# Performance work log

Hardware: AMD Instinct MI355X
Metric: run time of the kernel (lower is better)

## Reference

```python
import jax, jax.numpy as jnp
import numpy as np

HIDDEN = 1024
NUM_HEADS = 16
HEAD_DIM = HIDDEN // NUM_HEADS
GRID_SIZE = 5
SPLINE_ORDER = 3
NUM_COEF = GRID_SIZE + SPLINE_ORDER  # 8


def make_grid(in_features):
    # efficient-kan default grid: range [-1, 1], extended by spline_order on each side
    h = 2.0 / GRID_SIZE
    g = jnp.arange(-SPLINE_ORDER, GRID_SIZE + SPLINE_ORDER + 1, dtype=jnp.float32) * h - 1.0
    return jnp.broadcast_to(g, (in_features, g.shape[0]))  # (in, G+2k+1)


def b_splines(x, grid):
    # x: (N, in); grid: (in, G+2k+1) -> bases (N, in, G+k)
    x = x[..., None]
    bases = ((x >= grid[:, :-1]) & (x < grid[:, 1:])).astype(x.dtype)
    for k in range(1, SPLINE_ORDER + 1):
        left = (x - grid[:, : -(k + 1)]) / (grid[:, k:-1] - grid[:, : -(k + 1)])
        right = (grid[:, k + 1 :] - x) / (grid[:, k + 1 :] - grid[:, 1:-k])
        bases = left * bases[..., :-1] + right * bases[..., 1:]
    return bases


def kan_linear(x, base_w, spline_w, spline_scaler):
    # x: (..., in); base_w: (out, in); spline_w: (out, in, C); spline_scaler: (out, in)
    in_f = x.shape[-1]
    x2 = x.reshape(-1, in_f)
    base = jax.nn.silu(x2) @ base_w.T
    bases = b_splines(x2, make_grid(in_f))                      # (N, in, C)
    sw = spline_w * spline_scaler[..., None]                    # (out, in, C)
    spline = bases.reshape(x2.shape[0], -1) @ sw.reshape(sw.shape[0], -1).T
    return (base + spline).reshape(*x.shape[:-1], base_w.shape[0])


def apply_rope(x):
    # x: (B, H, S, D); interleaved rotary (lucidrains convention), theta=10000
    d, s = x.shape[-1], x.shape[-2]
    inv_freq = 1.0 / (10000.0 ** (jnp.arange(0, d, 2, dtype=jnp.float32) / d))
    freqs = jnp.arange(s, dtype=jnp.float32)[:, None] * inv_freq[None, :]  # (S, d/2)
    cos = jnp.repeat(jnp.cos(freqs), 2, axis=-1)
    sin = jnp.repeat(jnp.sin(freqs), 2, axis=-1)
    x1, x2 = x[..., 0::2], x[..., 1::2]
    rot = jnp.stack((-x2, x1), axis=-1).reshape(x.shape)
    return x * cos + rot * sin


def setup_inputs() -> dict:
    key = jax.random.key(0)
    ks = jax.random.split(key, 10)
    B, S, H = 2, 2048, HIDDEN
    H3 = 3 * H
    scale = 0.02
    return {
        "q": jax.random.normal(ks[0], (B, S, H), jnp.float32),
        "k": jax.random.normal(ks[1], (B, S, H), jnp.float32),
        "v": jax.random.normal(ks[2], (B, S, H), jnp.float32),
        "attn_mask": jnp.zeros((S, S), jnp.float32),
        "qkv_base_w": jax.random.normal(ks[3], (H3, H3), jnp.float32) * scale,
        "qkv_spline_w": jax.random.normal(ks[4], (H3, H3, NUM_COEF), jnp.float32) * scale,
        "qkv_scaler": jnp.ones((H3, H3), jnp.float32),
        "out_base_w": jax.random.normal(ks[5], (H, H), jnp.float32) * scale,
        "out_spline_w": jax.random.normal(ks[6], (H, H, NUM_COEF), jnp.float32) * scale,
        "out_scaler": jnp.ones((H, H), jnp.float32),
    }


def reference(q, k, v, attn_mask, qkv_base_w, qkv_spline_w, qkv_scaler,
              out_base_w, out_spline_w, out_scaler):
    B, S, H = q.shape
    x = jnp.concatenate((q, k, v), axis=2)                       # (B, S, 3H)
    qkv = kan_linear(x, qkv_base_w, qkv_spline_w, qkv_scaler)    # (B, S, 3H)
    qkv = qkv.reshape(B, S, NUM_HEADS, 3 * HEAD_DIM).transpose(0, 2, 1, 3)
    queries, keys, values = jnp.split(qkv, 3, axis=-1)           # each (B, nh, S, hd)
    queries = apply_rope(queries)
    keys = apply_rope(keys)
    scores = jnp.einsum("bhqd,bhkd->bhqk", queries, keys) / (HEAD_DIM ** 0.5) + attn_mask
    attention = jax.nn.softmax(scores, axis=-1)
    context = jnp.einsum("bhqk,bhkd->bhqd", attention, values)
    context = context.transpose(0, 2, 1, 3).reshape(B, S, H)
    return kan_linear(context, out_base_w, out_spline_w, out_scaler)
```

## Files before the change

### kernel.cpp

```cpp
#include <hip/hip_runtime.h>
#include <hip/hip_bf16.h>
#include <stdint.h>

typedef __bf16 bf16;
typedef __attribute__((ext_vector_type(8))) __bf16 bf16x8;
typedef __attribute__((ext_vector_type(4))) float f32x4;

#define DEVI __device__ __forceinline__

constexpr int BATCH = 2, SEQ = 2048, HID = 1024, NHEAD = 16, HDIM = 64;
constexpr int H3 = 3072;
constexpr int MROWS = BATCH * SEQ;
constexpr int KEXP = 9;
constexpr int K1DIM = H3 * KEXP;
constexpr int K2DIM = HID * KEXP;

constexpr size_t WQ_OFF  = 0;
constexpr size_t AQ_OFF  = 169869312;
constexpr size_t CQ_OFF  = AQ_OFF + 226492416;
constexpr size_t QR_OFF  = CQ_OFF + 50331648;
constexpr size_t KR_OFF  = QR_OFF + 8388608;
constexpr size_t VB_OFF  = KR_OFF + 8388608;
constexpr size_t CTX_OFF = VB_OFF + 8388608;
constexpr size_t A2_OFF  = 0;
constexpr size_t W2_OFF  = 75497472;

DEVI void gld_lds16(const void* g, void* l) {
  __builtin_amdgcn_global_load_lds((const __attribute__((address_space(1))) void*)g,
                                   (__attribute__((address_space(3))) void*)l, 16, 0, 0);
}

DEVI void silu_bases(float x, float* o9) {
  o9[0] = x / (1.0f + __expf(-x));
  float g[12];
#pragma unroll
  for (int j = 0; j < 12; ++j) g[j] = (float)(j - 3) * 0.4f - 1.0f;
  float b[11];
#pragma unroll
  for (int j = 0; j < 11; ++j) b[j] = (x >= g[j] && x < g[j + 1]) ? 1.0f : 0.0f;
#pragma unroll
  for (int k = 1; k <= 3; ++k) {
    const float inv = (k == 1) ? 2.5f : (k == 2) ? 1.25f : (1.0f / 1.2f);
#pragma unroll
    for (int j = 0; j + k < 11; ++j) {
      b[j] = (x - g[j]) * inv * b[j] + (g[j + k + 1] - x) * inv * b[j + 1];
    }
  }
#pragma unroll
  for (int c = 0; c < 8; ++c) o9[1 + c] = b[c];
}

__global__ void wprep_kernel(const float* __restrict__ bw, const float* __restrict__ sw,
                             const float* __restrict__ sc, bf16* __restrict__ W, int KK) {
  int i = blockIdx.x * blockDim.x + threadIdx.x;
  int n = blockIdx.y;
  if (i >= KK) return;
  size_t idx = (size_t)n * KK + i;
  float base = bw[idx];
  float scal = sc[idx];
  const float4* sp = (const float4*)(sw + idx * 8);
  float4 s0 = sp[0], s1 = sp[1];
  bf16* o = W + idx * KEXP;
  o[0] = (bf16)base;
  o[1] = (bf16)(s0.x * scal); o[2] = (bf16)(s0.y * scal);
  o[3] = (bf16)(s0.z * scal); o[4] = (bf16)(s0.w * scal);
  o[5] = (bf16)(s1.x * scal); o[6] = (bf16)(s1.y * scal);
  o[7] = (bf16)(s1.z * scal); o[8] = (bf16)(s1.w * scal);
}

__global__ void act_qkv_kernel(const float* __restrict__ qin, const float* __restrict__ kin,
                               const float* __restrict__ vin, bf16* __restrict__ A) {
  int i = blockIdx.x * blockDim.x + threadIdx.x;
  int m = blockIdx.y;
  int which = i >> 10, off = i & 1023;
  const float* src = (which == 0) ? qin : (which == 1) ? kin : vin;
  float x = src[(size_t)m * HID + off];
  float o9[9];
  silu_bases(x, o9);
  bf16* o = A + (size_t)m * K1DIM + (size_t)i * KEXP;
#pragma unroll
  for (int c = 0; c < 9; ++c) o[c] = (bf16)o9[c];
}

__global__ void act_out_kernel(const float* __restrict__ ctx, bf16* __restrict__ A) {
  int i = blockIdx.x * blockDim.x + threadIdx.x;
  int m = blockIdx.y;
  float x = ctx[(size_t)m * HID + i];
  float o9[9];
  silu_bases(x, o9);
  bf16* o = A + (size_t)m * K2DIM + (size_t)i * KEXP;
#pragma unroll
  for (int c = 0; c < 9; ++c) o[c] = (bf16)o9[c];
}

__global__ __launch_bounds__(256, 2)
void gemm_kernel(const bf16* __restrict__ A, const bf16* __restrict__ Bw,
                 float* __restrict__ C, int N, int K) {
  __shared__ bf16 As[128 * 64];
  __shared__ bf16 Bs[128 * 64];
  const int tid = threadIdx.x;
  const int lane = tid & 63;
  const int l15 = lane & 15, lq = lane >> 4;
  const int wid = tid >> 6;
  const int wm = (wid >> 1) * 64, wn = (wid & 1) * 64;
  const int bm = blockIdx.y, bn = blockIdx.x;
  f32x4 acc[4][4] = {};
  const int srow = tid >> 3;
  const int schk = (tid & 7) ^ (srow & 7);
  const bf16* aB = A + (size_t)(bm * 128 + srow) * K + schk * 8;
  const bf16* bB = Bw + (size_t)(bn * 128 + srow) * K + schk * 8;

  int aoff[2][4], boff[2][4];
#pragma unroll
  for (int ks = 0; ks < 2; ++ks) {
#pragma unroll
    for (int f = 0; f < 4; ++f) {
      int arow = wm + f * 16 + l15;
      int brow = wn + f * 16 + l15;
      aoff[ks][f] = arow * 64 + (((ks * 4 + lq) ^ (arow & 7)) * 8);
      boff[ks][f] = brow * 64 + (((ks * 4 + lq) ^ (brow & 7)) * 8);
    }
  }

  for (int kt = 0; kt < K; kt += 64) {
#pragma unroll
    for (int r = 0; r < 4; ++r) {
      gld_lds16(aB + (size_t)(r * 32) * K + kt, As + r * 2048 + tid * 8);
      gld_lds16(bB + (size_t)(r * 32) * K + kt, Bs + r * 2048 + tid * 8);
    }
    __syncthreads();
#pragma unroll
    for (int ks = 0; ks < 2; ++ks) {
      bf16x8 af[4], bfr[4];
#pragma unroll
      for (int mf = 0; mf < 4; ++mf)
        af[mf] = *(const bf16x8*)&As[aoff[ks][mf]];
#pragma unroll
      for (int nf = 0; nf < 4; ++nf)
        bfr[nf] = *(const bf16x8*)&Bs[boff[ks][nf]];
#pragma unroll
      for (int mf = 0; mf < 4; ++mf)
#pragma unroll
        for (int nf = 0; nf < 4; ++nf)
          acc[mf][nf] = __builtin_amdgcn_mfma_f32_16x16x32_bf16(af[mf], bfr[nf], acc[mf][nf], 0, 0, 0);
    }
    __syncthreads();
  }
#pragma unroll
  for (int mf = 0; mf < 4; ++mf)
#pragma unroll
    for (int nf = 0; nf < 4; ++nf)
#pragma unroll
      for (int r = 0; r < 4; ++r) {
        int row = bm * 128 + wm + mf * 16 + lq * 4 + r;
        int col = bn * 128 + wn + nf * 16 + l15;
        C[(size_t)row * N + col] = acc[mf][nf][r];
      }
}

__global__ void rope_kernel(const float* __restrict__ Cq, bf16* __restrict__ qr,
                            bf16* __restrict__ kr, bf16* __restrict__ vb) {
  int idx = blockIdx.x * blockDim.x + threadIdx.x;
  int p = idx & 31;
  int h = (idx >> 5) & 15;
  int m = idx >> 9;
  int s = m & (SEQ - 1);
  int b = m >> 11;
  const float* row = Cq + (size_t)m * H3 + h * 192;
  float q0 = row[2 * p], q1 = row[2 * p + 1];
  float k0 = row[64 + 2 * p], k1 = row[64 + 2 * p + 1];
  float v0 = row[128 + 2 * p], v1 = row[128 + 2 * p + 1];
  float invf = expf(-(float)p * (9.210340371976184f / 32.0f));
  float fr = (float)s * invf;
  float sn, cs;
  sincosf(fr, &sn, &cs);
  size_t o = (((size_t)(b * NHEAD + h)) * SEQ + s) * 64 + 2 * p;
  qr[o] = (bf16)(q0 * cs - q1 * sn); qr[o + 1] = (bf16)(q1 * cs + q0 * sn);
  kr[o] = (bf16)(k0 * cs - k1 * sn); kr[o + 1] = (bf16)(k1 * cs + k0 * sn);
  vb[o] = (bf16)v0; vb[o + 1] = (bf16)v1;
}

__global__ __launch_bounds__(256, 2)
void attn_kernel(const bf16* __restrict__ qr, const bf16* __restrict__ kr,
                 const bf16* __restrict__ vb, const float* __restrict__ mask,
                 float* __restrict__ ctx) {
  __shared__ bf16 Kt[64 * 64];
  __shared__ bf16 Vt[64 * 64];
  __shared__ bf16 Pl[4][16 * 64];
  const int tid = threadIdx.x, lane = tid & 63, wid = tid >> 6;
  const int l15 = lane & 15, lq = lane >> 4;
  const int qt = blockIdx.x, bh = blockIdx.y;
  const int b = bh >> 4, hh = bh & 15;
  const size_t baseQ = ((size_t)bh * SEQ + qt * 64 + wid * 16) * 64;
  bf16x8 aq[2];
  aq[0] = *(const bf16x8*)&qr[baseQ + (size_t)l15 * 64 + 0 + lq * 8];
  aq[1] = *(const bf16x8*)&qr[baseQ + (size_t)l15 * 64 + 32 + lq * 8];
  float mrow[4], lrow[4];
  f32x4 oacc[4] = {};
#pragma unroll
  for (int r = 0; r < 4; ++r) { mrow[r] = -1e30f; lrow[r] = 0.0f; }
  const float scale = 0.125f;
  for (int kv0 = 0; kv0 < SEQ; kv0 += 64) {
    const bf16* kBase = kr + ((size_t)bh * SEQ + kv0 + (tid >> 3)) * 64 + (tid & 7) * 8;
#pragma unroll
    for (int r = 0; r < 2; ++r)
      gld_lds16(kBase + (size_t)(r * 32) * 64, Kt + r * 2048 + tid * 8);
#pragma unroll
    for (int r = 0; r < 2; ++r) {
      int row = r * 32 + (tid >> 3);
      int c8 = (tid & 7) * 8;
      bf16x8 vv = *(const bf16x8*)&vb[((size_t)bh * SEQ + kv0 + row) * 64 + c8];
#pragma unroll
      for (int e = 0; e < 8; ++e) Vt[(c8 + e) * 64 + row] = vv[e];
    }
    __syncthreads();
    f32x4 sacc[4] = {};
#pragma unroll
    for (int k0 = 0; k0 < 2; ++k0) {
#pragma unroll
      for (int nf = 0; nf < 4; ++nf) {
        bf16x8 bk = *(const bf16x8*)&Kt[(nf * 16 + l15) * 64 + k0 * 32 + lq * 8];
        sacc[nf] = __builtin_amdgcn_mfma_f32_16x16x32_bf16(aq[k0], bk, sacc[nf], 0, 0, 0);
      }
    }
    const int qg0 = qt * 64 + wid * 16 + lq * 4;
#pragma unroll
    for (int nf = 0; nf < 4; ++nf) {
      int kvg = kv0 + nf * 16 + l15;
#pragma unroll
      for (int r = 0; r < 4; ++r)
        sacc[nf][r] = sacc[nf][r] * scale + mask[(size_t)(qg0 + r) * SEQ + kvg];
    }
    float fac[4];
#pragma unroll
    for (int r = 0; r < 4; ++r) {
      float v = fmaxf(fmaxf(sacc[0][r], sacc[1][r]), fmaxf(sacc[2][r], sacc[3][r]));
      v = fmaxf(v, __shfl_xor(v, 1));
      v = fmaxf(v, __shfl_xor(v, 2));
      v = fmaxf(v, __shfl_xor(v, 4));
      v = fmaxf(v, __shfl_xor(v, 8));
      float mnew = fmaxf(mrow[r], v);
      fac[r] = __expf(mrow[r] - mnew);
      mrow[r] = mnew;
    }
    float rs[4] = {0, 0, 0, 0};
#pragma unroll
    for (int nf = 0; nf < 4; ++nf)
#pragma unroll
      for (int r = 0; r < 4; ++r) {
        float pv = __expf(sacc[nf][r] - mrow[r]);
        sacc[nf][r] = pv;
        rs[r] += pv;
      }
#pragma unroll
    for (int r = 0; r < 4; ++r) {
      float v = rs[r];
      v += __shfl_xor(v, 1); v += __shfl_xor(v, 2);
      v += __shfl_xor(v, 4); v += __shfl_xor(v, 8);
      lrow[r] = lrow[r] * fac[r] + v;
    }
#pragma unroll
    for (int nf = 0; nf < 4; ++nf)
#pragma unroll
      for (int r = 0; r < 4; ++r)
        Pl[wid][(lq * 4 + r) * 64 + nf * 16 + l15] = (bf16)sacc[nf][r];
#pragma unroll
    for (int nf = 0; nf < 4; ++nf)
#pragma unroll
      for (int r = 0; r < 4; ++r)
        oacc[nf][r] *= fac[r];
#pragma unroll
    for (int k0 = 0; k0 < 2; ++k0) {
      bf16x8 ap = *(const bf16x8*)&Pl[wid][l15 * 64 + k0 * 32 + lq * 8];
#pragma unroll
      for (int nf = 0; nf < 4; ++nf) {
        bf16x8 bv = *(const bf16x8*)&Vt[(nf * 16 + l15) * 64 + k0 * 32 + lq * 8];
        oacc[nf] = __builtin_amdgcn_mfma_f32_16x16x32_bf16(ap, bv, oacc[nf], 0, 0, 0);
      }
    }
    __syncthreads();
  }
#pragma unroll
  for (int nf = 0; nf < 4; ++nf)
#pragma unroll
    for (int r = 0; r < 4; ++r) {
      int row = qt * 64 + wid * 16 + lq * 4 + r;
      int col = hh * 64 + nf * 16 + l15;
      ctx[((size_t)b * SEQ + row) * HID + col] = oacc[nf][r] / lrow[r];
    }
}

extern "C" void kernel_launch(void* const* d_in, const int* in_sizes, int n_in,
                              void* d_out, int out_size, void* d_ws, size_t ws_size,
                              hipStream_t stream) {
  const float* qin    = (const float*)d_in[0];
  const float* kin    = (const float*)d_in[1];
  const float* vin    = (const float*)d_in[2];
  const float* mask   = (const float*)d_in[3];
  const float* qkv_bw = (const float*)d_in[4];
  const float* qkv_sw = (const float*)d_in[5];
  const float* qkv_sc = (const float*)d_in[6];
  const float* out_bw = (const float*)d_in[7];
  const float* out_sw = (const float*)d_in[8];
  const float* out_sc = (const float*)d_in[9];
  char* ws = (char*)d_ws;
  bf16* Wq  = (bf16*)(ws + WQ_OFF);
  bf16* Aq  = (bf16*)(ws + AQ_OFF);
  float* Cq = (float*)(ws + CQ_OFF);
  bf16* qr  = (bf16*)(ws + QR_OFF);
  bf16* kr  = (bf16*)(ws + KR_OFF);
  bf16* vb  = (bf16*)(ws + VB_OFF);
  float* ctx = (float*)(ws + CTX_OFF);
  bf16* A2  = (bf16*)(ws + A2_OFF);
  bf16* W2  = (bf16*)(ws + W2_OFF);

  wprep_kernel<<<dim3(H3 / 256, H3), 256, 0, stream>>>(qkv_bw, qkv_sw, qkv_sc, Wq, H3);
  act_qkv_kernel<<<dim3(H3 / 256, MROWS), 256, 0, stream>>>(qin, kin, vin, Aq);
  gemm_kernel<<<dim3(H3 / 128, MROWS / 128), 256, 0, stream>>>(Aq, Wq, Cq, H3, K1DIM);
  rope_kernel<<<(MROWS * NHEAD * 32) / 256, 256, 0, stream>>>(Cq, qr, kr, vb);
  attn_kernel<<<dim3(SEQ / 64, BATCH * NHEAD), 256, 0, stream>>>(qr, kr, vb, mask, ctx);
  act_out_kernel<<<dim3(HID / 256, MROWS), 256, 0, stream>>>(ctx, A2);
  wprep_kernel<<<dim3(HID / 256, HID), 256, 0, stream>>>(out_bw, out_sw, out_sc, W2, HID);
  gemm_kernel<<<dim3(HID / 128, MROWS / 128), 256, 0, stream>>>(A2, W2, (float*)d_out, HID, K2DIM);
}
```

Baseline: 1.233 ms.

## Stage expanded activations/weights through LDS, raise GEMM occupancy, swizzle block order

The weight-prep and activation-expansion kernels now write their 9-element bf16 outputs into shared memory first, then store them to global memory as coalesced 16-byte vectors instead of scattered 2-byte stores. The GEMM launch bound is raised from 2 to 4 blocks per SM. Block indices are remapped so that consecutive hardware block IDs spread across groups of 8, aiming at better cache locality across XCDs. The higher occupancy target may force register spills in the GEMM, and the swizzle assumes the block count divides evenly by 8.

```diff
diff --git a/kernel.cpp b/kernel.cpp
--- a/kernel.cpp
+++ b/kernel.cpp
@@ -50,50 +50,74 @@
   for (int c = 0; c < 8; ++c) o9[1 + c] = b[c];
 }
 
-__global__ void wprep_kernel(const float* __restrict__ bw, const float* __restrict__ sw,
-                             const float* __restrict__ sc, bf16* __restrict__ W, int KK) {
-  int i = blockIdx.x * blockDim.x + threadIdx.x;
-  int n = blockIdx.y;
-  if (i >= KK) return;
-  size_t idx = (size_t)n * KK + i;
+__global__ __launch_bounds__(256)
+void wprep_kernel(const float* __restrict__ bw, const float* __restrict__ sw,
+                  const float* __restrict__ sc, bf16* __restrict__ W, int KK) {
+  __shared__ bf16 buf[256 * KEXP];
+  const int tid = threadIdx.x;
+  const int n = blockIdx.y;
+  const int i0 = blockIdx.x * 256;
+  const size_t idx = (size_t)n * KK + i0 + tid;
   float base = bw[idx];
   float scal = sc[idx];
   const float4* sp = (const float4*)(sw + idx * 8);
   float4 s0 = sp[0], s1 = sp[1];
-  bf16* o = W + idx * KEXP;
+  bf16* o = buf + tid * KEXP;
   o[0] = (bf16)base;
   o[1] = (bf16)(s0.x * scal); o[2] = (bf16)(s0.y * scal);
   o[3] = (bf16)(s0.z * scal); o[4] = (bf16)(s0.w * scal);
   o[5] = (bf16)(s1.x * scal); o[6] = (bf16)(s1.y * scal);
   o[7] = (bf16)(s1.z * scal); o[8] = (bf16)(s1.w * scal);
-}
-
-__global__ void act_qkv_kernel(const float* __restrict__ qin, const float* __restrict__ kin,
-                               const float* __restrict__ vin, bf16* __restrict__ A) {
-  int i = blockIdx.x * blockDim.x + threadIdx.x;
-  int m = blockIdx.y;
-  int which = i >> 10, off = i & 1023;
+  __syncthreads();
+  bf16* dst = W + (size_t)n * KK * KEXP + (size_t)i0 * KEXP;
+#pragma unroll
+  for (int j = tid; j < 256 * KEXP / 8; j += 256)
+    *(bf16x8*)(dst + j * 8) = *(const bf16x8*)(buf + j * 8);
+}
+
+__global__ __launch_bounds__(256)
+void act_qkv_kernel(const float* __restrict__ qin, const float* __restrict__ kin,
+                    const float* __restrict__ vin, bf16* __restrict__ A) {
+  __shared__ bf16 buf[256 * KEXP];
+  const int tid = threadIdx.x;
+  const int m = blockIdx.y;
+  const int i0 = blockIdx.x * 256;
+  const int i = i0 + tid;
+  const int which = i >> 10, off = i & 1023;
   const float* src = (which == 0) ? qin : (which == 1) ? kin : vin;
   float x = src[(size_t)m * HID + off];
   float o9[9];
   silu_bases(x, o9);
-  bf16* o = A + (size_t)m * K1DIM + (size_t)i * KEXP;
+  bf16* o = buf + tid * KEXP;
 #pragma unroll
   for (int c = 0; c < 9; ++c) o[c] = (bf16)o9[c];
-}
-
-__global__ void act_out_kernel(const float* __restrict__ ctx, bf16* __restrict__ A) {
-  int i = blockIdx.x * blockDim.x + threadIdx.x;
-  int m = blockIdx.y;
-  float x = ctx[(size_t)m * HID + i];
+  __syncthreads();
+  bf16* dst = A + (size_t)m * K1DIM + (size_t)i0 * KEXP;
+#pragma unroll
+  for (int j = tid; j < 256 * KEXP / 8; j += 256)
+    *(bf16x8*)(dst + j * 8) = *(const bf16x8*)(buf + j * 8);
+}
+
+__global__ __launch_bounds__(256)
+void act_out_kernel(const float* __restrict__ ctx, bf16* __restrict__ A) {
+  __shared__ bf16 buf[256 * KEXP];
+  const int tid = threadIdx.x;
+  const int m = blockIdx.y;
+  const int i0 = blockIdx.x * 256;
+  float x = ctx[(size_t)m * HID + i0 + tid];
   float o9[9];
   silu_bases(x, o9);
-  bf16* o = A + (size_t)m * K2DIM + (size_t)i * KEXP;
+  bf16* o = buf + tid * KEXP;
 #pragma unroll
   for (int c = 0; c < 9; ++c) o[c] = (bf16)o9[c];
-}
-
-__global__ __launch_bounds__(256, 2)
+  __syncthreads();
+  bf16* dst = A + (size_t)m * K2DIM + (size_t)i0 * KEXP;
+#pragma unroll
+  for (int j = tid; j < 256 * KEXP / 8; j += 256)
+    *(bf16x8*)(dst + j * 8) = *(const bf16x8*)(buf + j * 8);
+}
+
+__global__ __launch_bounds__(256, 4)
 void gemm_kernel(const bf16* __restrict__ A, const bf16* __restrict__ Bw,
                  float* __restrict__ C, int N, int K) {
   __shared__ bf16 As[128 * 64];
@@ -103,7 +127,12 @@
   const int l15 = lane & 15, lq = lane >> 4;
   const int wid = tid >> 6;
   const int wm = (wid >> 1) * 64, wn = (wid & 1) * 64;
-  const int bm = blockIdx.y, bn = blockIdx.x;
+  const int gx = gridDim.x;
+  const int nwg = gx * gridDim.y;
+  const int orig = blockIdx.y * gx + blockIdx.x;
+  const int swz = (orig & 7) * (nwg >> 3) + (orig >> 3);
+  const int bm = swz / gx;
+  const int bn = swz % gx;
   f32x4 acc[4][4] = {};
   const int srow = tid >> 3;
   const int schk = (tid & 7) ^ (srow & 7);
```

New measurement: 1.247 ms. About the same (+1.1%).
